# Kernel optimization log

Hardware: AMD Instinct MI355X
Metric: run time of the kernel (lower is better)

Reference implementation:

```python
import jax, jax.numpy as jnp
import numpy as np

N_NEURON = 500_000
N_EDGE = 10_000_000
TAO_D = 2.0
TAO_R = 10.0
DT = 0.1
LAMDA_D = DT / TAO_D  # dt/tao_d
LAMDA_R = DT / TAO_R  # dt/tao_r


def setup_inputs() -> dict:
    key = jax.random.key(0)
    ks = jax.random.split(key, 8)
    edges = jax.random.randint(ks[0], (2, N_EDGE), 0, N_NEURON, dtype=jnp.int64)  # row0=post, row1=pre
    return {
        "weight": jax.random.normal(ks[1], (N_EDGE,), dtype=jnp.float32),
        "edges": edges,
        "Iback": jax.random.normal(ks[2], (N_NEURON,), dtype=jnp.float32),
        "spike": jax.random.uniform(ks[3], (N_NEURON,), dtype=jnp.float32),
        "s": jax.random.normal(ks[4], (N_NEURON,), dtype=jnp.float32),
        "r": jax.random.normal(ks[5], (N_NEURON,), dtype=jnp.float32),
        "noise": jax.random.normal(ks[6], (N_NEURON,), dtype=jnp.float32),
        "dt_over_tau": jax.random.uniform(ks[7], (1,), dtype=jnp.float32),
        "sqrt_coeff": jnp.ones((1,), dtype=jnp.float32),
        "sig": jnp.ones((1,), dtype=jnp.float32),
        "mu": jnp.zeros((1,), dtype=jnp.float32),
    }


def reference(weight, edges, Iback, spike, s, r, noise, dt_over_tau, sqrt_coeff, sig, mu):
    # OU background-current update + effective input current
    Iback_new = Iback + dt_over_tau * (noise - Iback)
    Ieff = Iback_new / sqrt_coeff * sig + mu
    # dual-exponential synaptic trace updates
    s_new = s + LAMDA_R * (-s + spike / TAO_D)
    r_new = r - LAMDA_D * r + DT * s_new
    # sparse COO matvec: I[post] += w_e * r_new[pre]
    post, pre = edges[0], edges[1]
    I = jax.ops.segment_sum(weight * r_new[pre], post, num_segments=N_NEURON) + Ieff
    return I
```

## Files before the change

kernel.cpp:

```cpp
#include <hip/hip_runtime.h>
#include <hip/hip_fp16.h>

#define N_NEURON 500000
#define N_EDGE   10000000

#define DT_C      0.1f
#define LAMDA_D_C 0.05f
#define LAMDA_R_C 0.01f
#define INV_TAO_D 0.5f

#define BUCKET_SHIFT 11
#define BUCKET_W     (1 << BUCKET_SHIFT)
#define NBUCKET      ((N_NEURON + BUCKET_W - 1) >> BUCKET_SHIFT)

#define P1_BLOCK 512
#define P1_EPT   16
#define P1_CHUNK (P1_BLOCK * P1_EPT)
#define NCHUNK   ((N_EDGE + P1_CHUNK - 1) / P1_CHUNK)
#define OFFS_STRIDE 256
#define META_NONE 0xFFFFFFFFu

#define WS_RNEW_OFF  0u
#define WS_OFFS_OFF  (2u * 1024u * 1024u)
#define WS_REC_OFF   (4u * 1024u * 1024u)
#define WS_NEEDED    ((size_t)WS_REC_OFF + (size_t)NCHUNK * P1_CHUNK * 4u)

__device__ __forceinline__ unsigned pack_rec(int post, float v) {
    const unsigned short hv = __half_as_ushort(__float2half_rn(v));
    return ((unsigned)hv << 16) | ((unsigned)post & (BUCKET_W - 1));
}
__device__ __forceinline__ float rec_val(unsigned rec) {
    return __half2float(__ushort_as_half((unsigned short)(rec >> 16)));
}

__global__ void neuron_update_r(const float4* __restrict__ spike,
                                const float4* __restrict__ s,
                                const float4* __restrict__ r,
                                float4* __restrict__ r_new,
                                int n4) {
    const int i = blockIdx.x * blockDim.x + threadIdx.x;
    if (i >= n4) return;
    const float4 sv = s[i], sp = spike[i], rv = r[i];
    float4 rn;
    float sn;
    sn = sv.x + LAMDA_R_C * (-sv.x + sp.x * INV_TAO_D); rn.x = rv.x - LAMDA_D_C * rv.x + DT_C * sn;
    sn = sv.y + LAMDA_R_C * (-sv.y + sp.y * INV_TAO_D); rn.y = rv.y - LAMDA_D_C * rv.y + DT_C * sn;
    sn = sv.z + LAMDA_R_C * (-sv.z + sp.z * INV_TAO_D); rn.z = rv.z - LAMDA_D_C * rv.z + DT_C * sn;
    sn = sv.w + LAMDA_R_C * (-sv.w + sp.w * INV_TAO_D); rn.w = rv.w - LAMDA_D_C * rv.w + DT_C * sn;
    r_new[i] = rn;
}

__global__ __launch_bounds__(P1_BLOCK, 8) void edge_bin(
        const float* __restrict__ weight,
        const int*   __restrict__ post_arr,
        const int*   __restrict__ pre_arr,
        const float* __restrict__ r_new,
        unsigned*    __restrict__ records,
        unsigned*    __restrict__ offs,
        int n_edge) {
    __shared__ unsigned rec_lds[P1_CHUNK];
    __shared__ unsigned cnt[NBUCKET];
    __shared__ unsigned lbase[NBUCKET + 1];

    const int t      = threadIdx.x;
    const int chunk0 = blockIdx.x * P1_CHUNK;

    for (int i = t; i < NBUCKET; i += P1_BLOCK) cnt[i] = 0;
    __syncthreads();

    unsigned rec[P1_EPT];
    unsigned meta[P1_EPT];

    #pragma unroll
    for (int k = 0; k < P1_EPT / 4; ++k) {
        const int e = chunk0 + (k * P1_BLOCK + t) * 4;
        if (e < n_edge) {
            const int4   p4 = *reinterpret_cast<const int4*>(post_arr + e);
            const int4   q4 = *reinterpret_cast<const int4*>(pre_arr + e);
            const float4 w4 = *reinterpret_cast<const float4*>(weight + e);
            const int   ps[4] = {p4.x, p4.y, p4.z, p4.w};
            const int   qs[4] = {q4.x, q4.y, q4.z, q4.w};
            const float wv[4] = {w4.x, w4.y, w4.z, w4.w};
            #pragma unroll
            for (int j = 0; j < 4; ++j) {
                const unsigned b = ((unsigned)ps[j]) >> BUCKET_SHIFT;
                const unsigned l = atomicAdd(&cnt[b], 1u);
                rec[k * 4 + j]  = pack_rec(ps[j], wv[j] * r_new[qs[j]]);
                meta[k * 4 + j] = (b << 13) | l;
            }
        } else {
            #pragma unroll
            for (int j = 0; j < 4; ++j) meta[k * 4 + j] = META_NONE;
        }
    }
    __syncthreads();

    if (t < 64) {
        unsigned carry = 0;
        #pragma unroll
        for (int c = 0; c < 4; ++c) {
            const int idx = c * 64 + t;
            unsigned v = (idx < NBUCKET) ? cnt[idx] : 0u;
            const unsigned orig = v;
            #pragma unroll
            for (int d = 1; d < 64; d <<= 1) {
                const unsigned u = __shfl_up(v, d);
                if (t >= d) v += u;
            }
            if (idx <= NBUCKET) lbase[idx] = carry + v - orig;
            carry += __shfl(v, 63);
        }
    }
    __syncthreads();

    #pragma unroll
    for (int k = 0; k < P1_EPT; ++k) {
        if (meta[k] != META_NONE)
            rec_lds[lbase[meta[k] >> 13] + (meta[k] & 0x1FFFu)] = rec[k];
    }
    __syncthreads();

    if (t <= NBUCKET)
        offs[blockIdx.x * OFFS_STRIDE + t] = lbase[t];
    const unsigned total = lbase[NBUCKET];
    unsigned* dst = records + (size_t)blockIdx.x * P1_CHUNK;
    for (unsigned i = t; i < total; i += P1_BLOCK)
        dst[i] = rec_lds[i];
}

__global__ __launch_bounds__(1024) void bucket_reduce(
        const unsigned* __restrict__ records,
        const unsigned* __restrict__ offs,
        const float* __restrict__ Iback,
        const float* __restrict__ noise,
        const float* __restrict__ dt_over_tau,
        const float* __restrict__ sqrt_coeff,
        const float* __restrict__ sig,
        const float* __restrict__ mu,
        float*          __restrict__ out,
        int n, int nchunk) {
    __shared__ float acc[BUCKET_W];
    const int b = blockIdx.x;
    const int t = threadIdx.x;
    for (int i = t; i < BUCKET_W; i += 1024) acc[i] = 0.f;
    __syncthreads();

    const int grp = t >> 5, lane = t & 31;
    for (int j = grp; j < nchunk; j += 32) {
        const unsigned s0 = offs[j * OFFS_STRIDE + b];
        const unsigned e0 = offs[j * OFFS_STRIDE + b + 1];
        const unsigned* src = records + (size_t)j * P1_CHUNK;
        for (unsigned i = s0 + lane; i < e0; i += 32) {
            const unsigned rec = src[i];
            atomicAdd(&acc[rec & (BUCKET_W - 1)], rec_val(rec));
        }
    }
    __syncthreads();

    const float dtau = dt_over_tau[0];
    const float sq   = sqrt_coeff[0];
    const float sg   = sig[0];
    const float m    = mu[0];
    const int g0 = b << BUCKET_SHIFT;
    for (int i = t; i < BUCKET_W; i += 1024) {
        const int g = g0 + i;
        if (g < n) {
            const float ib   = Iback[g];
            const float ibn  = ib + dtau * (noise[g] - ib);
            out[g] = acc[i] + (ibn / sq * sg + m);
        }
    }
}

__global__ void neuron_update_full(const float* __restrict__ Iback,
                                   const float* __restrict__ spike,
                                   const float* __restrict__ s,
                                   const float* __restrict__ r,
                                   const float* __restrict__ noise,
                                   const float* __restrict__ dt_over_tau,
                                   const float* __restrict__ sqrt_coeff,
                                   const float* __restrict__ sig,
                                   const float* __restrict__ mu,
                                   float* __restrict__ r_new,
                                   float* __restrict__ out,
                                   int n) {
    const float dtau = dt_over_tau[0], sq = sqrt_coeff[0], sg = sig[0], m = mu[0];
    for (int i = blockIdx.x * blockDim.x + threadIdx.x; i < n;
         i += gridDim.x * blockDim.x) {
        float ib  = Iback[i];
        float ibn = ib + dtau * (noise[i] - ib);
        float sv  = s[i];
        float sn  = sv + LAMDA_R_C * (-sv + spike[i] * INV_TAO_D);
        float rv  = r[i];
        r_new[i] = rv - LAMDA_D_C * rv + DT_C * sn;
        out[i]   = ibn / sq * sg + m;
    }
}

__global__ void edge_scatter(const float* __restrict__ weight,
                             const int* __restrict__ post,
                             const int* __restrict__ pre,
                             const float* __restrict__ r_new,
                             float* __restrict__ out,
                             int n_edge) {
    for (int e = blockIdx.x * blockDim.x + threadIdx.x; e < n_edge;
         e += gridDim.x * blockDim.x) {
        atomicAdd(&out[post[e]], weight[e] * r_new[pre[e]]);
    }
}

extern "C" void kernel_launch(void* const* d_in, const int* in_sizes, int n_in,
                              void* d_out, int out_size, void* d_ws, size_t ws_size,
                              hipStream_t stream) {
    const float* weight      = (const float*)d_in[0];
    const int*   edges       = (const int*)d_in[1];
    const float* Iback       = (const float*)d_in[2];
    const float* spike       = (const float*)d_in[3];
    const float* s           = (const float*)d_in[4];
    const float* r           = (const float*)d_in[5];
    const float* noise       = (const float*)d_in[6];
    const float* dt_over_tau = (const float*)d_in[7];
    const float* sqrt_coeff  = (const float*)d_in[8];
    const float* sig         = (const float*)d_in[9];
    const float* mu          = (const float*)d_in[10];

    float* out = (float*)d_out;
    char*  ws  = (char*)d_ws;

    float*    r_new   = (float*)(ws + WS_RNEW_OFF);
    unsigned* offs    = (unsigned*)(ws + WS_OFFS_OFF);
    unsigned* records = (unsigned*)(ws + WS_REC_OFF);

    const int n_edge = in_sizes[0];
    const int n      = out_size;

    const int nchunk = (n_edge + P1_CHUNK - 1) / P1_CHUNK;

    if (ws_size >= WS_NEEDED) {
        {
            const int n4 = n / 4;
            neuron_update_r<<<(n4 + 255) / 256, 256, 0, stream>>>(
                (const float4*)spike, (const float4*)s, (const float4*)r,
                (float4*)r_new, n4);
        }
        edge_bin<<<nchunk, P1_BLOCK, 0, stream>>>(
            weight, edges, edges + n_edge, r_new, records, offs, n_edge);

        bucket_reduce<<<NBUCKET, 1024, 0, stream>>>(
            records, offs, Iback, noise, dt_over_tau, sqrt_coeff, sig, mu,
            out, n, nchunk);
    } else {
        neuron_update_full<<<(n + 255) / 256, 256, 0, stream>>>(
            Iback, spike, s, r, noise, dt_over_tau, sqrt_coeff, sig, mu,
            r_new, out, n);
        edge_scatter<<<4096, 256, 0, stream>>>(
            weight, edges, edges + n_edge, r_new, out, n_edge);
    }
}
```

Measured before the change: 121.7 us.

## Double edge_bin chunk size with two-pass count then scatter binning

Doubles the edges per block in the binning kernel and restructures it into two passes. The first pass reads only post indices to build per-bucket counts, and the second rereads post, pre and weight in two halves to gather r_new and scatter records into shared memory. This drops the per-edge register arrays for records and metadata, which allows a larger chunk, halves the number of blocks and chunks the reduce kernel walks, and batches the r_new gathers. In exchange the post array is read twice, occupancy is lowered via launch bounds, and there is an extra round of shared-memory atomics.

Result: slower. 140.1 us (+15.1%).

```diff
diff --git a/kernel.cpp b/kernel.cpp
--- a/kernel.cpp
+++ b/kernel.cpp
@@ -14,11 +14,10 @@
 #define NBUCKET      ((N_NEURON + BUCKET_W - 1) >> BUCKET_SHIFT)
 
 #define P1_BLOCK 512
-#define P1_EPT   16
+#define P1_EPT   32
 #define P1_CHUNK (P1_BLOCK * P1_EPT)
 #define NCHUNK   ((N_EDGE + P1_CHUNK - 1) / P1_CHUNK)
 #define OFFS_STRIDE 256
-#define META_NONE 0xFFFFFFFFu
 
 #define WS_RNEW_OFF  0u
 #define WS_OFFS_OFF  (2u * 1024u * 1024u)
@@ -50,7 +49,7 @@
     r_new[i] = rn;
 }
 
-__global__ __launch_bounds__(P1_BLOCK, 8) void edge_bin(
+__global__ __launch_bounds__(P1_BLOCK, 4) void edge_bin(
         const float* __restrict__ weight,
         const int*   __restrict__ post_arr,
         const int*   __restrict__ pre_arr,
@@ -68,29 +67,22 @@
     for (int i = t; i < NBUCKET; i += P1_BLOCK) cnt[i] = 0;
     __syncthreads();
 
-    unsigned rec[P1_EPT];
-    unsigned meta[P1_EPT];
-
-    #pragma unroll
-    for (int k = 0; k < P1_EPT / 4; ++k) {
-        const int e = chunk0 + (k * P1_BLOCK + t) * 4;
-        if (e < n_edge) {
-            const int4   p4 = *reinterpret_cast<const int4*>(post_arr + e);
-            const int4   q4 = *reinterpret_cast<const int4*>(pre_arr + e);
-            const float4 w4 = *reinterpret_cast<const float4*>(weight + e);
-            const int   ps[4] = {p4.x, p4.y, p4.z, p4.w};
-            const int   qs[4] = {q4.x, q4.y, q4.z, q4.w};
-            const float wv[4] = {w4.x, w4.y, w4.z, w4.w};
-            #pragma unroll
-            for (int j = 0; j < 4; ++j) {
-                const unsigned b = ((unsigned)ps[j]) >> BUCKET_SHIFT;
-                const unsigned l = atomicAdd(&cnt[b], 1u);
-                rec[k * 4 + j]  = pack_rec(ps[j], wv[j] * r_new[qs[j]]);
-                meta[k * 4 + j] = (b << 13) | l;
-            }
-        } else {
-            #pragma unroll
-            for (int j = 0; j < 4; ++j) meta[k * 4 + j] = META_NONE;
+    {
+        int4 P[8];
+        #pragma unroll
+        for (int k = 0; k < 8; ++k) {
+            const int e = chunk0 + (k * P1_BLOCK + t) * 4;
+            P[k] = (e < n_edge) ? *reinterpret_cast<const int4*>(post_arr + e)
+                                : make_int4(-1, -1, -1, -1);
+        }
+        #pragma unroll
+        for (int k = 0; k < 8; ++k) {
+            if (P[k].x >= 0) {
+                atomicAdd(&cnt[((unsigned)P[k].x) >> BUCKET_SHIFT], 1u);
+                atomicAdd(&cnt[((unsigned)P[k].y) >> BUCKET_SHIFT], 1u);
+                atomicAdd(&cnt[((unsigned)P[k].z) >> BUCKET_SHIFT], 1u);
+                atomicAdd(&cnt[((unsigned)P[k].w) >> BUCKET_SHIFT], 1u);
+            }
         }
     }
     __syncthreads();
@@ -113,10 +105,47 @@
     }
     __syncthreads();
 
+    for (int i = t; i < NBUCKET; i += P1_BLOCK) cnt[i] = 0;
+    __syncthreads();
+
     #pragma unroll
-    for (int k = 0; k < P1_EPT; ++k) {
-        if (meta[k] != META_NONE)
-            rec_lds[lbase[meta[k] >> 13] + (meta[k] & 0x1FFFu)] = rec[k];
+    for (int h = 0; h < 2; ++h) {
+        int4   P[4], Q[4];
+        float4 W[4];
+        #pragma unroll
+        for (int k = 0; k < 4; ++k) {
+            const int e = chunk0 + ((h * 4 + k) * P1_BLOCK + t) * 4;
+            if (e < n_edge) {
+                P[k] = *reinterpret_cast<const int4*>(post_arr + e);
+                Q[k] = *reinterpret_cast<const int4*>(pre_arr + e);
+                W[k] = *reinterpret_cast<const float4*>(weight + e);
+            } else {
+                P[k] = make_int4(-1, -1, -1, -1);
+                Q[k] = make_int4(0, 0, 0, 0);
+                W[k] = make_float4(0.f, 0.f, 0.f, 0.f);
+            }
+        }
+        float g[16];
+        #pragma unroll
+        for (int k = 0; k < 4; ++k) {
+            g[k * 4 + 0] = r_new[Q[k].x];
+            g[k * 4 + 1] = r_new[Q[k].y];
+            g[k * 4 + 2] = r_new[Q[k].z];
+            g[k * 4 + 3] = r_new[Q[k].w];
+        }
+        #pragma unroll
+        for (int k = 0; k < 4; ++k) {
+            const int   ps[4] = {P[k].x, P[k].y, P[k].z, P[k].w};
+            const float wv[4] = {W[k].x, W[k].y, W[k].z, W[k].w};
+            #pragma unroll
+            for (int j = 0; j < 4; ++j) {
+                if (ps[j] >= 0) {
+                    const unsigned b = ((unsigned)ps[j]) >> BUCKET_SHIFT;
+                    const unsigned l = atomicAdd(&cnt[b], 1u);
+                    rec_lds[lbase[b] + l] = pack_rec(ps[j], wv[j] * g[k * 4 + j]);
+                }
+            }
+        }
     }
     __syncthreads();
 
@@ -165,8 +194,8 @@
     for (int i = t; i < BUCKET_W; i += 1024) {
         const int g = g0 + i;
         if (g < n) {
-            const float ib   = Iback[g];
-            const float ibn  = ib + dtau * (noise[g] - ib);
+            const float ib  = Iback[g];
+            const float ibn = ib + dtau * (noise[g] - ib);
             out[g] = acc[i] + (ibn / sq * sg + m);
         }
     }
```
